# Performance work log

Hardware: AMD Instinct MI355X
Metric: run time of the kernel (lower is better)

The kernel has to match this reference:

```python
import jax, jax.numpy as jnp
from jax import lax
import numpy as np

N = 1024           # num_nodes
E = 32768          # edges per hop adjacency (avg degree 32)
EMB, HID, REP = 128, 64, 32
PATH_LENGTHS = (2, 3)


def _conv2d(x, w, b, pad):
    y = lax.conv_general_dilated(x, w, (1, 1), [(pad, pad), (pad, pad)],
                                 dimension_numbers=('NCHW', 'OIHW', 'NCHW'))
    return y + b[None, :, None, None]


def _tconv2d(x, w, b):
    # ConvTranspose2d(kernel=2, stride=2, pad=0) == conv with lhs_dilation=2, pad=1 (out = 2*in)
    y = lax.conv_general_dilated(x, w, (1, 1), [(1, 1), (1, 1)],
                                 lhs_dilation=(2, 2),
                                 dimension_numbers=('NCHW', 'OIHW', 'NCHW'))
    return y + b[None, :, None, None]


def _maxpool2(x):
    return lax.reduce_window(x, -jnp.inf, lax.max, (1, 1, 2, 2), (1, 1, 2, 2), 'VALID')


def _att_block(a, p):
    # ConvEncoder: conv->pool->conv->pool->tconv->tconv, relu/relu/relu/sigmoid
    h = jax.nn.relu(_conv2d(a, p[0], p[1], 1))
    h = _maxpool2(h)
    h = jax.nn.relu(_conv2d(h, p[2], p[3], 2))
    h = _maxpool2(h)
    h = jax.nn.relu(_tconv2d(h, p[4], p[5]))
    return jax.nn.sigmoid(_tconv2d(h, p[6], p[7]))


def _dense_gcn_norm(A):
    # add_remaining_self_loops(fill=1) + D^{-1/2} A D^{-1/2}; deg = row-sum (scatter_add over row)
    A = A + jnp.diag(jnp.where(jnp.diagonal(A) == 0, 1.0, 0.0).astype(A.dtype))
    deg = A.sum(axis=1)
    safe = jnp.where(deg > 0, deg, 1.0)
    dinv = jnp.where(deg > 0, lax.rsqrt(safe), 0.0)
    return dinv[:, None] * A * dinv[None, :]


def _edges_to_dense(e):
    # torch.sparse.FloatTensor(idx, ones).to_dense() sums duplicate edges
    return jnp.zeros((N, N), jnp.float32).at[e[0], e[1]].add(1.0)


def _path_transform(adjs, p):
    # adjs: [L, N, N] dense per-hop adjacencies of one meta-path
    att = _att_block(adjs[None], p)[0][:, :N, :N]
    attended = adjs * att
    M = jnp.eye(N, dtype=adjs.dtype)
    for i in range(adjs.shape[0]):  # fixed small loop over hops
        M = _dense_gcn_norm(M @ attended[i])
    return M


def _forward(x, p0, p1, w1, bias1, w2, bias2, e00, e01, e10, e11, e12):
    A0 = jnp.stack([_edges_to_dense(e00), _edges_to_dense(e01)])
    A1 = jnp.stack([_edges_to_dense(e10), _edges_to_dense(e11), _edges_to_dense(e12)])
    M0 = _path_transform(A0, p0)
    M1 = _path_transform(A1, p1)
    A = jnp.maximum(M0, M1)  # coalesce(op='max') over union; values are >= 0
    An = _dense_gcn_norm(A)  # GCNConv internal normalization (same for both layers)
    h = jax.nn.relu(An @ (x @ w1) + bias1)
    # dropout inactive (eval mode)
    return An @ (h @ w2) + bias2


def setup_inputs():
    key = jax.random.key(0)
    ks = iter(jax.random.split(key, 40))
    d = {}
    d['x'] = jax.random.normal(next(ks), (N, EMB), jnp.float32)
    d['mp0_e0'] = jax.random.randint(next(ks), (2, E), 0, N)
    d['mp0_e1'] = jax.random.randint(next(ks), (2, E), 0, N)
    d['mp1_e0'] = jax.random.randint(next(ks), (2, E), 0, N)
    d['mp1_e1'] = jax.random.randint(next(ks), (2, E), 0, N)
    d['mp1_e2'] = jax.random.randint(next(ks), (2, E), 0, N)
    for bi, L in enumerate(PATH_LENGTHS):
        pre = 'b%d_' % bi
        d[pre + 'c1w'] = jax.random.normal(next(ks), (16, L, 3, 3), jnp.float32) * 0.1
        d[pre + 'c1b'] = jnp.zeros((16,), jnp.float32)
        d[pre + 'c2w'] = jax.random.normal(next(ks), (4, 16, 3, 3), jnp.float32) * 0.1
        d[pre + 'c2b'] = jnp.zeros((4,), jnp.float32)
        d[pre + 't1w'] = jax.random.normal(next(ks), (16, 4, 2, 2), jnp.float32) * 0.1
        d[pre + 't1b'] = jnp.zeros((16,), jnp.float32)
        d[pre + 't2w'] = jax.random.normal(next(ks), (L, 16, 2, 2), jnp.float32) * 0.1
        d[pre + 't2b'] = jnp.zeros((L,), jnp.float32)
    d['w1'] = jax.random.normal(next(ks), (EMB, HID), jnp.float32) * (1.0 / np.sqrt(EMB)).astype(np.float32)
    d['bias1'] = jnp.zeros((HID,), jnp.float32)
    d['w2'] = jax.random.normal(next(ks), (HID, REP), jnp.float32) * (1.0 / np.sqrt(HID)).astype(np.float32)
    d['bias2'] = jnp.zeros((REP,), jnp.float32)
    return d


def reference(x, mp0_e0, mp0_e1, mp1_e0, mp1_e1, mp1_e2,
              b0_c1w, b0_c1b, b0_c2w, b0_c2b, b0_t1w, b0_t1b, b0_t2w, b0_t2b,
              b1_c1w, b1_c1b, b1_c2w, b1_c2b, b1_t1w, b1_t1b, b1_t2w, b1_t2b,
              w1, bias1, w2, bias2):
    p0 = (b0_c1w, b0_c1b, b0_c2w, b0_c2b, b0_t1w, b0_t1b, b0_t2w, b0_t2b)
    p1 = (b1_c1w, b1_c1b, b1_c2w, b1_c2b, b1_t1w, b1_t1b, b1_t2w, b1_t2b)
    return _forward(x, p0, p1, w1, bias1, w2, bias2,
                    mp0_e0, mp0_e1, mp1_e0, mp1_e1, mp1_e2)
```

## Files before the change

### kernel.cpp

```cpp
#include <hip/hip_runtime.h>
#include <math.h>

#define N 1024
#define NN (N*N)
#define NE 32768

#define OFF_A    ((size_t)0)
#define OFF_H10  ((size_t)(5*NN))
#define OFF_M0   ((size_t)(5*NN))
#define OFF_CSR  ((size_t)(7*NN))
#define OFF_BT   ((size_t)(9*NN))
#define OFF_M1   ((size_t)(10*NN))
#define OFF_AN   ((size_t)(11*NN))
#define OFF_H20  ((size_t)(13*NN))
#define OFF_H21  (OFF_H20 + 264196)
#define OFF_SC   (OFF_H21 + 264196)
#define SC_D0a 0
#define SC_F0a 1024
#define SC_D1a 2048
#define SC_F1a 3072
#define SC_D0b 4096
#define SC_F0b 5120
#define SC_D1b 6144
#define SC_F1b 7168
#define SC_D1c 8192
#define SC_F1c 9216
#define SC_D2  10240
#define SC_F2  11264
#define SC_DEG 12288
#define SC_DGV 13312
#define OFF_XW1  (OFF_SC + 14336)
#define OFF_HB   (OFF_XW1 + 65536)
#define OFF_HW2  (OFF_HB + 65536)

#define CSR_STRIDE 96
#define CSRF (1024 * CSR_STRIDE)
#define CSC_MAXT 80

__global__ void k_scatter5(const int* __restrict__ e0, const int* __restrict__ e1,
                           const int* __restrict__ e2, const int* __restrict__ e3,
                           const int* __restrict__ e4, float* __restrict__ A) {
  int g = blockIdx.x * 256 + threadIdx.x;
  int seg = g >> 15;
  int k = g & 32767;
  const int* e = (seg == 0) ? e0 : (seg == 1) ? e1 : (seg == 2) ? e2 : (seg == 3) ? e3 : e4;
  atomicAdd(&A[(size_t)seg * NN + (size_t)e[k] * N + e[NE + k]], 1.0f);
}

template<int L>
__device__ __forceinline__ void conv1_body(const float* __restrict__ A,
    const float* __restrict__ W, const float* __restrict__ Bn, float* __restrict__ out) {
  __shared__ float sIn[L][34][35];
  __shared__ float sW[16 * L * 9];
  __shared__ float sB[16];
  int tid = threadIdx.y * 16 + threadIdx.x;
  for (int i = tid; i < 16 * L * 9; i += 256) sW[i] = W[i];
  if (tid < 16) sB[tid] = Bn[tid];
  const int x0 = blockIdx.x * 32 - 1;
  const int y0 = blockIdx.y * 32 - 1;
  for (int idx = tid; idx < L * 34 * 34; idx += 256) {
    int l = idx / (34 * 34);
    int rem = idx - l * 34 * 34;
    int r = rem / 34, c = rem - r * 34;
    int iy = y0 + r, ix = x0 + c;
    sIn[l][r][c] = (iy >= 0 && iy < N && ix >= 0 && ix < N) ? A[(size_t)l * NN + (size_t)iy * N + ix] : 0.f;
  }
  __syncthreads();
  const int tx = threadIdx.x, ty = threadIdx.y;
  float p[L][4][4];
  #pragma unroll
  for (int l = 0; l < L; ++l)
    #pragma unroll
    for (int r = 0; r < 4; ++r)
      #pragma unroll
      for (int c = 0; c < 4; ++c)
        p[l][r][c] = sIn[l][2 * ty + r][2 * tx + c];
  const int ox = blockIdx.x * 16 + tx;
  const int oy = blockIdx.y * 16 + ty;
  for (int oc = 0; oc < 16; ++oc) {
    float wr[L * 9];
    #pragma unroll
    for (int t = 0; t < L * 9; ++t) wr[t] = sW[oc * L * 9 + t];
    float m = -1e30f;
    #pragma unroll
    for (int dy = 0; dy < 2; ++dy)
      #pragma unroll
      for (int dx = 0; dx < 2; ++dx) {
        float s = 0.f;
        #pragma unroll
        for (int l = 0; l < L; ++l)
          #pragma unroll
          for (int ky = 0; ky < 3; ++ky)
            #pragma unroll
            for (int kx = 0; kx < 3; ++kx)
              s = fmaf(p[l][dy + ky][dx + kx], wr[l * 9 + ky * 3 + kx], s);
        m = fmaxf(m, s);
      }
    out[(size_t)oc * 262144 + (size_t)oy * 512 + ox] = fmaxf(m + sB[oc], 0.f);
  }
}

__global__ __launch_bounds__(256) void k_conv1_both(const float* __restrict__ Ab,
    const float* __restrict__ W0, const float* __restrict__ b0,
    const float* __restrict__ W1, const float* __restrict__ b1, float* __restrict__ H1b) {
  if (blockIdx.z == 0) conv1_body<2>(Ab, W0, b0, H1b);
  else                 conv1_body<3>(Ab + 2 * NN, W1, b1, H1b + 4 * NN);
}

__global__ __launch_bounds__(256) void k_conv2_both(const float* __restrict__ H1b,
    const float* __restrict__ W0, const float* __restrict__ b0,
    const float* __restrict__ W1, const float* __restrict__ b1,
    float* __restrict__ H2_0, float* __restrict__ H2_1) {
  const int z = blockIdx.z;
  const float* in = H1b + (size_t)z * 4 * NN;
  const float* W  = z ? W1 : W0;
  const float* Bn = z ? b1 : b0;
  float* out = z ? H2_1 : H2_0;
  __shared__ float sW[4 * 16 * 9];
  __shared__ float sB[4];
  const int tid = threadIdx.x;
  for (int i = tid; i < 576; i += 256) sW[i] = W[i];
  if (tid < 4) sB[tid] = Bn[tid];
  __syncthreads();
  const int tx = tid & 15, ty = tid >> 4;
  const int ox = blockIdx.x * 16 + tx;
  const int oy = blockIdx.y * 16 + ty;
  if (ox >= 257 || oy >= 257) return;
  const int x0 = 2 * ox - 2;
  const int y0 = 2 * oy - 2;
  const bool c0ok = (x0 >= 0);
  const bool c1ok = (x0 + 2 < 512);
  float acc[4][2][2];
  #pragma unroll
  for (int oc = 0; oc < 4; ++oc)
    #pragma unroll
    for (int dy = 0; dy < 2; ++dy)
      #pragma unroll
      for (int dx = 0; dx < 2; ++dx) acc[oc][dy][dx] = 0.f;
  for (int ic = 0; ic < 16; ++ic) {
    const float* base = in + (size_t)ic * 262144;
    float p[4][4];
    #pragma unroll
    for (int r = 0; r < 4; ++r) {
      const int iy = y0 + r;
      const bool rowok = (iy >= 0 && iy < 512);
      float2 a = make_float2(0.f, 0.f), b = make_float2(0.f, 0.f);
      if (rowok) {
        const float* rp = base + (size_t)iy * 512;
        if (c0ok) a = *(const float2*)(rp + x0);
        if (c1ok) b = *(const float2*)(rp + x0 + 2);
      }
      p[r][0] = a.x; p[r][1] = a.y; p[r][2] = b.x; p[r][3] = b.y;
    }
    #pragma unroll
    for (int oc = 0; oc < 4; ++oc) {
      float wr[9];
      #pragma unroll
      for (int t = 0; t < 9; ++t) wr[t] = sW[oc * 144 + ic * 9 + t];
      #pragma unroll
      for (int ky = 0; ky < 3; ++ky)
        #pragma unroll
        for (int kx = 0; kx < 3; ++kx) {
          const float w = wr[ky * 3 + kx];
          #pragma unroll
          for (int dy = 0; dy < 2; ++dy)
            #pragma unroll
            for (int dx = 0; dx < 2; ++dx)
              acc[oc][dy][dx] = fmaf(p[dy + ky][dx + kx], w, acc[oc][dy][dx]);
        }
    }
  }
  #pragma unroll
  for (int oc = 0; oc < 4; ++oc) {
    float m = fmaxf(fmaxf(acc[oc][0][0], acc[oc][0][1]), fmaxf(acc[oc][1][0], acc[oc][1][1]));
    out[(size_t)oc * 66049 + (size_t)oy * 257 + ox] = fmaxf(m + sB[oc], 0.f);
  }
}

__global__ __launch_bounds__(256) void k_tc_both(
    const float* __restrict__ H2_0, const float* __restrict__ H2_1,
    const float* __restrict__ t1w0, const float* __restrict__ t1b0,
    const float* __restrict__ t2w0, const float* __restrict__ t2b0,
    const float* __restrict__ t1w1, const float* __restrict__ t1b1,
    const float* __restrict__ t2w1, const float* __restrict__ t2b1,
    float* __restrict__ Ab) {
  const int z = blockIdx.z;
  const int L = 2 + z;
  const float* in  = z ? H2_1 : H2_0;
  const float* W1p = z ? t1w1 : t1w0;
  const float* B1p = z ? t1b1 : t1b0;
  const float* W2p = z ? t2w1 : t2w0;
  const float* B2p = z ? t2b1 : t2b0;
  float* A = Ab + (size_t)z * 2 * NN;
  __shared__ float sW1[256], sB1[16], sW2[192], sB2[3];
  int tid = threadIdx.y * 16 + threadIdx.x;
  sW1[tid] = W1p[tid];
  if (tid < 16) sB1[tid] = B1p[tid];
  for (int i = tid; i < L * 64; i += 256) sW2[i] = W2p[i];
  if (tid < L) sB2[tid] = B2p[tid];
  __syncthreads();
  const int n = blockIdx.x * 16 + threadIdx.x;
  const int m = blockIdx.y * 16 + threadIdx.y;
  const int p = m >> 1, q = n >> 1;
  const int f1y = 1 - (m & 1), f1x = 1 - (n & 1);
  float vin[4];
  #pragma unroll
  for (int ci = 0; ci < 4; ++ci) vin[ci] = in[(size_t)ci * 66049 + (size_t)p * 257 + q];
  float v[16];
  #pragma unroll
  for (int c = 0; c < 16; ++c) {
    float s = sB1[c];
    #pragma unroll
    for (int ci = 0; ci < 4; ++ci)
      s = fmaf(vin[ci], sW1[c * 16 + ci * 4 + f1y * 2 + f1x], s);
    v[c] = fmaxf(s, 0.f);
  }
  for (int l = 0; l < L; ++l) {
    #pragma unroll
    for (int dy = 0; dy < 2; ++dy)
      #pragma unroll
      for (int dx = 0; dx < 2; ++dx) {
        float s = sB2[l];
        #pragma unroll
        for (int c = 0; c < 16; ++c)
          s = fmaf(v[c], sW2[l * 64 + c * 4 + (1 - dy) * 2 + (1 - dx)], s);
        float sg = 1.f / (1.f + expf(-s));
        size_t idx = (size_t)l * NN + (size_t)(2 * m + dy) * N + (2 * n + dx);
        A[idx] *= sg;
      }
  }
}

__global__ __launch_bounds__(256) void k_extract(const float* __restrict__ Ab,
    int* __restrict__ gcol, float* __restrict__ gval, int* __restrict__ gcnt,
    int* __restrict__ crowT, float* __restrict__ cvalT, int* __restrict__ ccnt,
    float* __restrict__ DEGACC,
    float* __restrict__ D0a, float* __restrict__ F0a,
    float* __restrict__ D1a, float* __restrict__ F1a) {
  const int row = blockIdx.x;
  const int y = blockIdx.y;
  const float* base = Ab + (size_t)y * NN + (size_t)row * N;
  __shared__ int cnt;
  __shared__ float sdiag;
  __shared__ float red[4];
  if (threadIdx.x == 0) cnt = 0;
  __syncthreads();
  const int j4 = threadIdx.x;
  float4 v = ((const float4*)base)[j4];
  if (j4 == (row >> 2)) sdiag = ((const float*)&v)[row & 3];
  if (y == 4) {
    if (threadIdx.x == 0) DEGACC[row] = 0.f;
    #pragma unroll
    for (int t = 0; t < 4; ++t) {
      float x = ((const float*)&v)[t];
      if (x != 0.f) {
        int j = 4 * j4 + t;
        int p = atomicAdd(&ccnt[j], 1);
        if (p < CSC_MAXT) { crowT[p * 1024 + j] = row; cvalT[p * 1024 + j] = x; }
      }
    }
    return;
  }
  const size_t rb = ((size_t)y * 1024 + row) * CSR_STRIDE;
  #pragma unroll
  for (int t = 0; t < 4; ++t) {
    float x = ((const float*)&v)[t];
    if (x != 0.f) {
      int p = atomicAdd(&cnt, 1);
      if (p < CSR_STRIDE) { gcol[rb + p] = 4 * j4 + t; gval[rb + p] = x; }
    }
  }
  float s = v.x + v.y + v.z + v.w;
  #pragma unroll
  for (int o = 32; o > 0; o >>= 1) s += __shfl_down(s, o, 64);
  if ((threadIdx.x & 63) == 0) red[threadIdx.x >> 6] = s;
  __syncthreads();
  if (threadIdx.x == 0) {
    gcnt[(size_t)y * 1024 + row] = (cnt < CSR_STRIDE) ? cnt : CSR_STRIDE;
    if (y == 0 || y == 2) {
      float tot = red[0] + red[1] + red[2] + red[3];
      float fl = (sdiag == 0.f) ? 1.f : 0.f;
      float deg = tot + fl;
      float* D = (y == 0) ? D0a : D1a;
      float* F = (y == 0) ? F0a : F1a;
      D[row] = (deg > 0.f) ? (1.f / sqrtf(deg)) : 0.f;
      F[row] = fl;
    }
  }
}

__global__ __launch_bounds__(256) void k_spmm(
    const int* __restrict__ gcol, const float* __restrict__ gval, const int* __restrict__ gcnt,
    const float* __restrict__ D0a, const float* __restrict__ F0a,
    const float* __restrict__ D1a, const float* __restrict__ F1a,
    float* __restrict__ M0, float* __restrict__ BT,
    float* __restrict__ D0b, float* __restrict__ F0b,
    float* __restrict__ D1b, float* __restrict__ F1b) {
  const int row = blockIdx.x;
  const int y = blockIdx.y;
  const int lm = y * 2, rm = y * 2 + 1;
  const float* Da = y ? D1a : D0a;
  const float* Fa = y ? F1a : F0a;
  __shared__ __align__(16) float acc[1024];
  __shared__ int lcol[112];
  __shared__ float lw[112];
  __shared__ int lrc[112];
  __shared__ int cl;
  __shared__ float red[4];
  __shared__ float sdiag;
  ((float4*)acc)[threadIdx.x] = make_float4(0.f, 0.f, 0.f, 0.f);
  const float di = Da[row];
  const int cnt_l = gcnt[(size_t)lm * 1024 + row];
  const size_t lb = ((size_t)lm * 1024 + row) * CSR_STRIDE;
  if (threadIdx.x < cnt_l) {
    int k = gcol[lb + threadIdx.x];
    lcol[threadIdx.x] = k;
    lw[threadIdx.x] = di * gval[lb + threadIdx.x] * Da[k];
    lrc[threadIdx.x] = gcnt[(size_t)rm * 1024 + k];
  }
  if (threadIdx.x == 0) {
    int c = cnt_l;
    if (Fa[row] != 0.f) {
      lcol[c] = row; lw[c] = di * di; lrc[c] = gcnt[(size_t)rm * 1024 + row]; ++c;
    }
    cl = c;
  }
  __syncthreads();
  const int sub = threadIdx.x >> 5, lane = threadIdx.x & 31;
  const int cle = cl;
  for (int e = sub; e < cle; e += 8) {
    const int k = lcol[e];
    const float w = lw[e];
    const int rc = lrc[e];
    const size_t rbv = ((size_t)rm * 1024 + k) * CSR_STRIDE;
    for (int t = lane; t < rc; t += 32)
      atomicAdd(&acc[gcol[rbv + t]], w * gval[rbv + t]);
  }
  __syncthreads();
  float4 o = ((const float4*)acc)[threadIdx.x];
  float* C = y ? BT : M0;
  ((float4*)(C + (size_t)row * N))[threadIdx.x] = o;
  if (threadIdx.x == (row >> 2)) sdiag = ((const float*)&o)[row & 3];
  float s = o.x + o.y + o.z + o.w;
  #pragma unroll
  for (int off = 32; off > 0; off >>= 1) s += __shfl_down(s, off, 64);
  if ((threadIdx.x & 63) == 0) red[threadIdx.x >> 6] = s;
  __syncthreads();
  if (threadIdx.x == 0) {
    float tot = red[0] + red[1] + red[2] + red[3];
    float fl = (sdiag == 0.f) ? 1.f : 0.f;
    float deg = tot + fl;
    float* D = y ? D1b : D0b;
    float* F = y ? F1b : F0b;
    D[row] = (deg > 0.f) ? (1.f / sqrtf(deg)) : 0.f;
    F[row] = fl;
  }
}

__global__ __launch_bounds__(256) void k_spmm2(const float* __restrict__ BT,
    const float* __restrict__ D1b, const float* __restrict__ F1b,
    const int* __restrict__ crowT, const float* __restrict__ cvalT, const int* __restrict__ ccnt,
    float* __restrict__ M1, float* __restrict__ DEGACC, float* __restrict__ DIAGV) {
  const int g0 = blockIdx.x << 3;
  const int j  = (blockIdx.y << 8) + threadIdx.x;
  __shared__ float bt[1024 * 9];
  __shared__ float wsum[4][8];
  const int tid = threadIdx.x;
  for (int kq = 0; kq < 4; ++kq) {
    const int k = (kq << 8) + tid;
    const float dv = D1b[k];
    #pragma unroll
    for (int row = 0; row < 8; ++row)
      bt[k * 9 + row] = BT[(size_t)(g0 + row) * N + k] * dv;
  }
  __syncthreads();
  if (tid < 8) {
    const int gr = g0 + tid;
    bt[gr * 9 + tid] += F1b[gr] * D1b[gr];
  }
  __syncthreads();
  int cn = ccnt[j];
  cn = min(cn, CSC_MAXT);
  float o[8];
  #pragma unroll
  for (int row = 0; row < 8; ++row) o[row] = 0.f;
  for (int t = 0; t < cn; ++t) {
    const int   r = crowT[t * 1024 + j];
    const float v = cvalT[t * 1024 + j];
    const int rb = r * 9;
    #pragma unroll
    for (int row = 0; row < 8; ++row)
      o[row] = fmaf(bt[rb + row], v, o[row]);
  }
  #pragma unroll
  for (int row = 0; row < 8; ++row) o[row] *= D1b[g0 + row];
  #pragma unroll
  for (int row = 0; row < 8; ++row)
    M1[(size_t)(g0 + row) * N + j] = o[row];
  if ((unsigned)(j - g0) < 8u) DIAGV[j] = o[j - g0];
  #pragma unroll
  for (int row = 0; row < 8; ++row) {
    float s = o[row];
    #pragma unroll
    for (int off = 32; off > 0; off >>= 1) s += __shfl_down(s, off, 64);
    if ((tid & 63) == 0) wsum[tid >> 6][row] = s;
  }
  __syncthreads();
  if (tid < 8) {
    float p = wsum[0][tid] + wsum[1][tid] + wsum[2][tid] + wsum[3][tid];
    atomicAdd(&DEGACC[g0 + tid], p);
  }
}

__global__ void k_fin(const float* __restrict__ DEGACC, const float* __restrict__ DIAGV,
                      float* __restrict__ D1c, float* __restrict__ F1c) {
  const int row = blockIdx.x * 256 + threadIdx.x;
  const float fl = (DIAGV[row] == 0.f) ? 1.f : 0.f;
  const float deg = DEGACC[row] + fl;
  D1c[row] = (deg > 0.f) ? (1.f / sqrtf(deg)) : 0.f;
  F1c[row] = fl;
}

__global__ __launch_bounds__(256) void k_maxdeg(const float* __restrict__ M0,
    const float* __restrict__ d0, const float* __restrict__ f0,
    const float* __restrict__ M1, const float* __restrict__ d1, const float* __restrict__ f1,
    float* __restrict__ Aout, float* __restrict__ dinv2, float* __restrict__ dflg2) {
  const int row = blockIdx.x;
  const int j4 = threadIdx.x;
  const float r0 = d0[row], r1 = d1[row];
  const float fl0 = f0[row], fl1 = f1[row];
  float4 a = ((const float4*)(M0 + (size_t)row * N))[j4];
  float4 b = ((const float4*)(M1 + (size_t)row * N))[j4];
  const float4 c0 = ((const float4*)d0)[j4];
  const float4 c1 = ((const float4*)d1)[j4];
  int d = row - 4 * j4;
  if ((unsigned)d < 4u) { ((float*)&a)[d] += fl0; ((float*)&b)[d] += fl1; }
  float4 o;
  o.x = fmaxf(a.x * r0 * c0.x, b.x * r1 * c1.x);
  o.y = fmaxf(a.y * r0 * c0.y, b.y * r1 * c1.y);
  o.z = fmaxf(a.z * r0 * c0.z, b.z * r1 * c1.z);
  o.w = fmaxf(a.w * r0 * c0.w, b.w * r1 * c1.w);
  ((float4*)(Aout + (size_t)row * N))[j4] = o;
  __shared__ float sdiag;
  if ((unsigned)d < 4u) sdiag = ((float*)&o)[d];
  float s = o.x + o.y + o.z + o.w;
  #pragma unroll
  for (int off = 32; off > 0; off >>= 1) s += __shfl_down(s, off, 64);
  __shared__ float red[4];
  if ((threadIdx.x & 63) == 0) red[threadIdx.x >> 6] = s;
  __syncthreads();
  if (threadIdx.x == 0) {
    float tot = red[0] + red[1] + red[2] + red[3];
    float fl = (sdiag == 0.0f) ? 1.0f : 0.0f;
    float deg = tot + fl;
    dinv2[row] = (deg > 0.0f) ? (1.0f / sqrtf(deg)) : 0.0f;
    dflg2[row] = fl;
  }
}

template<int K, int NCOL, bool BIAS, bool RELU>
__global__ void k_mm_small(const float* __restrict__ A, const float* __restrict__ B,
                           const float* __restrict__ bias, float* __restrict__ out) {
  const int j = threadIdx.x;
  const int i = blockIdx.x * blockDim.y + threadIdx.y;
  const float* ar = A + (size_t)i * K;
  float acc = 0.f;
  #pragma unroll 8
  for (int k = 0; k < K; ++k) acc = fmaf(ar[k], B[(size_t)k * NCOL + j], acc);
  if (BIAS) acc += bias[j];
  if (RELU) acc = fmaxf(acc, 0.f);
  out[(size_t)i * NCOL + j] = acc;
}

template<int NCOL, bool RELU>
__global__ void k_an_mm(const float* __restrict__ BT, const float* __restrict__ dinv,
                        const float* __restrict__ dflg, const float* __restrict__ Bm,
                        const float* __restrict__ bias, float* __restrict__ out) {
  const int j = threadIdx.x;
  const int i = blockIdx.x * blockDim.y + threadIdx.y;
  const float di = dinv[i];
  const float* ar = BT + (size_t)i * N;
  float acc = 0.f;
  for (int k = 0; k < N; k += 4) {
    float4 a4 = *(const float4*)&ar[k];
    float4 d4 = *(const float4*)&dinv[k];
    acc = fmaf(a4.x * d4.x, Bm[(size_t)(k + 0) * NCOL + j], acc);
    acc = fmaf(a4.y * d4.y, Bm[(size_t)(k + 1) * NCOL + j], acc);
    acc = fmaf(a4.z * d4.z, Bm[(size_t)(k + 2) * NCOL + j], acc);
    acc = fmaf(a4.w * d4.w, Bm[(size_t)(k + 3) * NCOL + j], acc);
  }
  acc = fmaf(dflg[i] * dinv[i], Bm[(size_t)i * NCOL + j], acc);
  acc = fmaf(di, acc, bias[j]);
  if (RELU) acc = fmaxf(acc, 0.f);
  out[(size_t)i * NCOL + j] = acc;
}

extern "C" void kernel_launch(void* const* d_in, const int* in_sizes, int n_in,
                              void* d_out, int out_size, void* d_ws, size_t ws_size,
                              hipStream_t stream) {
  const float* x     = (const float*)d_in[0];
  const float* w1    = (const float*)d_in[22];
  const float* bias1 = (const float*)d_in[23];
  const float* w2    = (const float*)d_in[24];
  const float* bias2 = (const float*)d_in[25];
  float* out = (float*)d_out;
  float* ws  = (float*)d_ws;

  float* A    = ws + OFF_A;
  float* H1   = ws + OFF_H10;
  float* M0   = ws + OFF_M0;
  float* BT   = ws + OFF_BT;
  float* M1   = ws + OFF_M1;
  float* AN   = ws + OFF_AN;
  float* H2_0 = ws + OFF_H20;
  float* H2_1 = ws + OFF_H21;
  int*   gcol  = (int*)(ws + OFF_CSR);
  float* gval  = ws + OFF_CSR + (size_t)4 * CSRF;
  int*   gcnt  = (int*)(ws + OFF_CSR + (size_t)8 * CSRF);
  int*   crowT = (int*)(ws + OFF_CSR + (size_t)8 * CSRF + 4096);
  float* cvalT = ws + OFF_CSR + (size_t)8 * CSRF + 4096 + CSC_MAXT * 1024;
  int*   ccnt  = (int*)(ws + OFF_CSR + (size_t)8 * CSRF + 4096 + (size_t)2 * CSC_MAXT * 1024);
  float* SC   = ws + OFF_SC;
  float *D0a = SC + SC_D0a, *F0a = SC + SC_F0a, *D1a = SC + SC_D1a, *F1a = SC + SC_F1a;
  float *D0b = SC + SC_D0b, *F0b = SC + SC_F0b, *D1b = SC + SC_D1b, *F1b = SC + SC_F1b;
  float *D1c = SC + SC_D1c, *F1c = SC + SC_F1c, *D2 = SC + SC_D2, *F2 = SC + SC_F2;
  float *DEGACC = SC + SC_DEG, *DIAGV = SC + SC_DGV;
  float* XW1 = ws + OFF_XW1;
  float* HB  = ws + OFF_HB;
  float* HW2 = ws + OFF_HW2;

  hipMemsetAsync(A, 0, (size_t)5 * NN * sizeof(float), stream);

  dim3 b256(256), b16(16, 16);
  k_mm_small<128, 64, false, false><<<256, dim3(64, 4), 0, stream>>>(x, w1, nullptr, XW1);

  k_scatter5<<<640, b256, 0, stream>>>((const int*)d_in[1], (const int*)d_in[2],
                                       (const int*)d_in[3], (const int*)d_in[4],
                                       (const int*)d_in[5], A);

  k_conv1_both<<<dim3(32, 32, 2), b16, 0, stream>>>(A,
      (const float*)d_in[6], (const float*)d_in[7],
      (const float*)d_in[14], (const float*)d_in[15], H1);
  k_conv2_both<<<dim3(17, 17, 2), b256, 0, stream>>>(H1,
      (const float*)d_in[8], (const float*)d_in[9],
      (const float*)d_in[16], (const float*)d_in[17], H2_0, H2_1);
  k_tc_both<<<dim3(32, 32, 2), b16, 0, stream>>>(H2_0, H2_1,
      (const float*)d_in[10], (const float*)d_in[11],
      (const float*)d_in[12], (const float*)d_in[13],
      (const float*)d_in[18], (const float*)d_in[19],
      (const float*)d_in[20], (const float*)d_in[21], A);

  hipMemsetAsync(ccnt, 0, 1024 * sizeof(int), stream);

  k_extract<<<dim3(1024, 5), b256, 0, stream>>>(A, gcol, gval, gcnt,
      crowT, cvalT, ccnt, DEGACC, D0a, F0a, D1a, F1a);

  k_spmm<<<dim3(1024, 2), b256, 0, stream>>>(gcol, gval, gcnt,
      D0a, F0a, D1a, F1a, M0, BT, D0b, F0b, D1b, F1b);

  k_spmm2<<<dim3(128, 4), b256, 0, stream>>>(BT, D1b, F1b, crowT, cvalT, ccnt,
                                             M1, DEGACC, DIAGV);
  k_fin<<<4, b256, 0, stream>>>(DEGACC, DIAGV, D1c, F1c);

  k_maxdeg<<<1024, b256, 0, stream>>>(M0, D0b, F0b, M1, D1c, F1c, AN, D2, F2);

  k_an_mm<64, true><<<256, dim3(64, 4), 0, stream>>>(AN, D2, F2, XW1, bias1, HB);
  k_mm_small<64, 32, false, false><<<128, dim3(32, 8), 0, stream>>>(HB, w2, nullptr, HW2);
  k_an_mm<32, false><<<128, dim3(32, 8), 0, stream>>>(AN, D2, F2, HW2, bias2, out);
}
```

Baseline: 369.1 us.

## Fuse sparse extraction into transposed-conv epilogue and merge small GEMM stages

The attention-apply kernel now emits CSR/CSC entries, degree sums and diagonals directly while multiplying the adjacency by the sigmoid attention. This removes the separate pass that re-read the five dense 1024x1024 matrices. Zeroing of the counters moves into the first conv block, which drops a memset. The final-norm kernel is folded into k_maxdeg, and the second hidden GEMM is fused with the layer-1 aggregation. The cost is global atomics per nonzero on the row counters and degree sums, and nondeterministic ordering inside each CSR row.

```diff
diff --git a/kernel.cpp b/kernel.cpp
--- a/kernel.cpp
+++ b/kernel.cpp
@@ -15,23 +15,26 @@
 #define OFF_H20  ((size_t)(13*NN))
 #define OFF_H21  (OFF_H20 + 264196)
 #define OFF_SC   (OFF_H21 + 264196)
-#define SC_D0a 0
-#define SC_F0a 1024
-#define SC_D1a 2048
-#define SC_F1a 3072
-#define SC_D0b 4096
-#define SC_F0b 5120
-#define SC_D1b 6144
-#define SC_F1b 7168
-#define SC_D1c 8192
-#define SC_F1c 9216
-#define SC_D2  10240
-#define SC_F2  11264
-#define SC_DEG 12288
-#define SC_DGV 13312
-#define OFF_XW1  (OFF_SC + 14336)
-#define OFF_HB   (OFF_XW1 + 65536)
-#define OFF_HW2  (OFF_HB + 65536)
+#define SC_D0a   0
+#define SC_F0a   1024
+#define SC_D1a   2048
+#define SC_F1a   3072
+#define SC_D0b   4096
+#define SC_F0b   5120
+#define SC_D1b   6144
+#define SC_F1b   7168
+#define SC_D2    8192
+#define SC_F2    9216
+#define SC_ZERO  10240
+#define SC_DEG   10240
+#define SC_GCNT  11264
+#define SC_CCNT  15360
+#define SC_DEGA  16384
+#define SC_DIAGA 18432
+#define SC_DGV   20480
+#define SC_END   21504
+#define OFF_XW1  (OFF_SC + SC_END)
+#define OFF_HW2  (OFF_XW1 + 65536)
 
 #define CSR_STRIDE 96
 #define CSRF (1024 * CSR_STRIDE)
@@ -102,7 +105,12 @@
 
 __global__ __launch_bounds__(256) void k_conv1_both(const float* __restrict__ Ab,
     const float* __restrict__ W0, const float* __restrict__ b0,
-    const float* __restrict__ W1, const float* __restrict__ b1, float* __restrict__ H1b) {
+    const float* __restrict__ W1, const float* __restrict__ b1,
+    float* __restrict__ H1b, float* __restrict__ ZC) {
+  if (blockIdx.x == 0 && blockIdx.y == 0 && blockIdx.z == 0) {
+    int tid = threadIdx.y * 16 + threadIdx.x;
+    for (int i = tid; i < 10240; i += 256) ZC[i] = 0.f;
+  }
   if (blockIdx.z == 0) conv1_body<2>(Ab, W0, b0, H1b);
   else                 conv1_body<3>(Ab + 2 * NN, W1, b1, H1b + 4 * NN);
 }
@@ -177,13 +185,16 @@
   }
 }
 
-__global__ __launch_bounds__(256) void k_tc_both(
+__global__ __launch_bounds__(256) void k_tc_emit(
     const float* __restrict__ H2_0, const float* __restrict__ H2_1,
     const float* __restrict__ t1w0, const float* __restrict__ t1b0,
     const float* __restrict__ t2w0, const float* __restrict__ t2b0,
     const float* __restrict__ t1w1, const float* __restrict__ t1b1,
     const float* __restrict__ t2w1, const float* __restrict__ t2b1,
-    float* __restrict__ Ab) {
+    const float* __restrict__ Ab,
+    int* __restrict__ gcolA, float* __restrict__ gvalA, int* __restrict__ gcntA,
+    int* __restrict__ crowT, float* __restrict__ cvalT, int* __restrict__ ccnt,
+    float* __restrict__ DEGA, float* __restrict__ DIAGA) {
   const int z = blockIdx.z;
   const int L = 2 + z;
   const float* in  = z ? H2_1 : H2_0;
@@ -191,7 +202,6 @@
   const float* B1p = z ? t1b1 : t1b0;
   const float* W2p = z ? t2w1 : t2w0;
   const float* B2p = z ? t2b1 : t2b0;
-  float* A = Ab + (size_t)z * 2 * NN;
   __shared__ float sW1[256], sB1[16], sW2[192], sB2[3];
   int tid = threadIdx.y * 16 + threadIdx.x;
   sW1[tid] = W1p[tid];
@@ -206,16 +216,17 @@
   float vin[4];
   #pragma unroll
   for (int ci = 0; ci < 4; ++ci) vin[ci] = in[(size_t)ci * 66049 + (size_t)p * 257 + q];
-  float v[16];
+  float v16[16];
   #pragma unroll
   for (int c = 0; c < 16; ++c) {
     float s = sB1[c];
     #pragma unroll
     for (int ci = 0; ci < 4; ++ci)
       s = fmaf(vin[ci], sW1[c * 16 + ci * 4 + f1y * 2 + f1x], s);
-    v[c] = fmaxf(s, 0.f);
+    v16[c] = fmaxf(s, 0.f);
   }
   for (int l = 0; l < L; ++l) {
+    const int mat = z * 2 + l;
     #pragma unroll
     for (int dy = 0; dy < 2; ++dy)
       #pragma unroll
@@ -223,70 +234,41 @@
         float s = sB2[l];
         #pragma unroll
         for (int c = 0; c < 16; ++c)
-          s = fmaf(v[c], sW2[l * 64 + c * 4 + (1 - dy) * 2 + (1 - dx)], s);
-        float sg = 1.f / (1.f + expf(-s));
-        size_t idx = (size_t)l * NN + (size_t)(2 * m + dy) * N + (2 * n + dx);
-        A[idx] *= sg;
+          s = fmaf(v16[c], sW2[l * 64 + c * 4 + (1 - dy) * 2 + (1 - dx)], s);
+        const float sg = 1.f / (1.f + expf(-s));
+        const int grow = 2 * m + dy, gc = 2 * n + dx;
+        const float av = Ab[(size_t)mat * NN + (size_t)grow * N + gc];
+        const float v = av * sg;
+        if (v != 0.f) {
+          if (mat == 4) {
+            int pp = atomicAdd(&ccnt[gc], 1);
+            if (pp < CSC_MAXT) { crowT[pp * 1024 + gc] = grow; cvalT[pp * 1024 + gc] = v; }
+          } else {
+            int pp = atomicAdd(&gcntA[mat * 1024 + grow], 1);
+            if (pp < CSR_STRIDE) {
+              size_t rb = ((size_t)mat * 1024 + grow) * CSR_STRIDE;
+              gcolA[rb + pp] = gc; gvalA[rb + pp] = v;
+            }
+          }
+          if (mat == 0 || mat == 2) {
+            atomicAdd(&DEGA[(mat >> 1) * 1024 + grow], v);
+            if (grow == gc) DIAGA[(mat >> 1) * 1024 + grow] = v;
+          }
+        }
       }
   }
 }
 
-__global__ __launch_bounds__(256) void k_extract(const float* __restrict__ Ab,
-    int* __restrict__ gcol, float* __restrict__ gval, int* __restrict__ gcnt,
-    int* __restrict__ crowT, float* __restrict__ cvalT, int* __restrict__ ccnt,
-    float* __restrict__ DEGACC,
+__global__ void k_finA(const float* __restrict__ DEGA, const float* __restrict__ DIAGA,
     float* __restrict__ D0a, float* __restrict__ F0a,
     float* __restrict__ D1a, float* __restrict__ F1a) {
-  const int row = blockIdx.x;
-  const int y = blockIdx.y;
-  const float* base = Ab + (size_t)y * NN + (size_t)row * N;
-  __shared__ int cnt;
-  __shared__ float sdiag;
-  __shared__ float red[4];
-  if (threadIdx.x == 0) cnt = 0;
-  __syncthreads();
-  const int j4 = threadIdx.x;
-  float4 v = ((const float4*)base)[j4];
-  if (j4 == (row >> 2)) sdiag = ((const float*)&v)[row & 3];
-  if (y == 4) {
-    if (threadIdx.x == 0) DEGACC[row] = 0.f;
-    #pragma unroll
-    for (int t = 0; t < 4; ++t) {
-      float x = ((const float*)&v)[t];
-      if (x != 0.f) {
-        int j = 4 * j4 + t;
-        int p = atomicAdd(&ccnt[j], 1);
-        if (p < CSC_MAXT) { crowT[p * 1024 + j] = row; cvalT[p * 1024 + j] = x; }
-      }
-    }
-    return;
-  }
-  const size_t rb = ((size_t)y * 1024 + row) * CSR_STRIDE;
-  #pragma unroll
-  for (int t = 0; t < 4; ++t) {
-    float x = ((const float*)&v)[t];
-    if (x != 0.f) {
-      int p = atomicAdd(&cnt, 1);
-      if (p < CSR_STRIDE) { gcol[rb + p] = 4 * j4 + t; gval[rb + p] = x; }
-    }
-  }
-  float s = v.x + v.y + v.z + v.w;
-  #pragma unroll
-  for (int o = 32; o > 0; o >>= 1) s += __shfl_down(s, o, 64);
-  if ((threadIdx.x & 63) == 0) red[threadIdx.x >> 6] = s;
-  __syncthreads();
-  if (threadIdx.x == 0) {
-    gcnt[(size_t)y * 1024 + row] = (cnt < CSR_STRIDE) ? cnt : CSR_STRIDE;
-    if (y == 0 || y == 2) {
-      float tot = red[0] + red[1] + red[2] + red[3];
-      float fl = (sdiag == 0.f) ? 1.f : 0.f;
-      float deg = tot + fl;
-      float* D = (y == 0) ? D0a : D1a;
-      float* F = (y == 0) ? F0a : F1a;
-      D[row] = (deg > 0.f) ? (1.f / sqrtf(deg)) : 0.f;
-      F[row] = fl;
-    }
-  }
+  const int i = blockIdx.x * 256 + threadIdx.x;
+  const int which = i >> 10, row = i & 1023;
+  const float fl = (DIAGA[i] == 0.f) ? 1.f : 0.f;
+  const float deg = DEGA[i] + fl;
+  const float d = (deg > 0.f) ? (1.f / sqrtf(deg)) : 0.f;
+  if (which == 0) { D0a[row] = d; F0a[row] = fl; }
+  else            { D1a[row] = d; F1a[row] = fl; }
 }
 
 __global__ __launch_bounds__(256) void k_spmm(
@@ -310,18 +292,19 @@
   __shared__ float sdiag;
   ((float4*)acc)[threadIdx.x] = make_float4(0.f, 0.f, 0.f, 0.f);
   const float di = Da[row];
-  const int cnt_l = gcnt[(size_t)lm * 1024 + row];
+  const int cnt_l = min(gcnt[(size_t)lm * 1024 + row], CSR_STRIDE);
   const size_t lb = ((size_t)lm * 1024 + row) * CSR_STRIDE;
   if (threadIdx.x < cnt_l) {
     int k = gcol[lb + threadIdx.x];
     lcol[threadIdx.x] = k;
     lw[threadIdx.x] = di * gval[lb + threadIdx.x] * Da[k];
-    lrc[threadIdx.x] = gcnt[(size_t)rm * 1024 + k];
+    lrc[threadIdx.x] = min(gcnt[(size_t)rm * 1024 + k], CSR_STRIDE);
   }
   if (threadIdx.x == 0) {
     int c = cnt_l;
     if (Fa[row] != 0.f) {
-      lcol[c] = row; lw[c] = di * di; lrc[c] = gcnt[(size_t)rm * 1024 + row]; ++c;
+      lcol[c] = row; lw[c] = di * di;
+      lrc[c] = min(gcnt[(size_t)rm * 1024 + row], CSR_STRIDE); ++c;
     }
     cl = c;
   }
@@ -412,27 +395,34 @@
   }
 }
 
-__global__ void k_fin(const float* __restrict__ DEGACC, const float* __restrict__ DIAGV,
-                      float* __restrict__ D1c, float* __restrict__ F1c) {
-  const int row = blockIdx.x * 256 + threadIdx.x;
-  const float fl = (DIAGV[row] == 0.f) ? 1.f : 0.f;
-  const float deg = DEGACC[row] + fl;
-  D1c[row] = (deg > 0.f) ? (1.f / sqrtf(deg)) : 0.f;
-  F1c[row] = fl;
-}
-
 __global__ __launch_bounds__(256) void k_maxdeg(const float* __restrict__ M0,
     const float* __restrict__ d0, const float* __restrict__ f0,
-    const float* __restrict__ M1, const float* __restrict__ d1, const float* __restrict__ f1,
+    const float* __restrict__ M1,
+    const float* __restrict__ DEGACC, const float* __restrict__ DIAGV,
     float* __restrict__ Aout, float* __restrict__ dinv2, float* __restrict__ dflg2) {
   const int row = blockIdx.x;
   const int j4 = threadIdx.x;
-  const float r0 = d0[row], r1 = d1[row];
-  const float fl0 = f0[row], fl1 = f1[row];
+  const float r0 = d0[row], fl0 = f0[row];
+  const float flr = (DIAGV[row] == 0.f) ? 1.f : 0.f;
+  const float degr = DEGACC[row] + flr;
+  const float r1 = (degr > 0.f) ? (1.f / sqrtf(degr)) : 0.f;
+  const float fl1 = flr;
   float4 a = ((const float4*)(M0 + (size_t)row * N))[j4];
   float4 b = ((const float4*)(M1 + (size_t)row * N))[j4];
   const float4 c0 = ((const float4*)d0)[j4];
-  const float4 c1 = ((const float4*)d1)[j4];
+  const float4 da = ((const float4*)DEGACC)[j4];
+  const float4 gv = ((const float4*)DIAGV)[j4];
+  float4 c1;
+  {
+    float fx = (gv.x == 0.f) ? 1.f : 0.f, dx_ = da.x + fx;
+    float fy = (gv.y == 0.f) ? 1.f : 0.f, dy_ = da.y + fy;
+    float fz = (gv.z == 0.f) ? 1.f : 0.f, dz_ = da.z + fz;
+    float fw = (gv.w == 0.f) ? 1.f : 0.f, dw_ = da.w + fw;
+    c1.x = (dx_ > 0.f) ? (1.f / sqrtf(dx_)) : 0.f;
+    c1.y = (dy_ > 0.f) ? (1.f / sqrtf(dy_)) : 0.f;
+    c1.z = (dz_ > 0.f) ? (1.f / sqrtf(dz_)) : 0.f;
+    c1.w = (dw_ > 0.f) ? (1.f / sqrtf(dw_)) : 0.f;
+  }
   int d = row - 4 * j4;
   if ((unsigned)d < 4u) { ((float*)&a)[d] += fl0; ((float*)&b)[d] += fl1; }
   float4 o;
@@ -470,6 +460,38 @@
   if (BIAS) acc += bias[j];
   if (RELU) acc = fmaxf(acc, 0.f);
   out[(size_t)i * NCOL + j] = acc;
+}
+
+__global__ void k_an_mm1(const float* __restrict__ AN, const float* __restrict__ dinv,
+                         const float* __restrict__ dflg, const float* __restrict__ XW1,
+                         const float* __restrict__ bias1, const float* __restrict__ w2,
+                         float* __restrict__ HW2) {
+  __shared__ float hsh[4][64];
+  const int j = threadIdx.x;
+  const int ty = threadIdx.y;
+  const int i = blockIdx.x * 4 + ty;
+  const float di = dinv[i];
+  const float* ar = AN + (size_t)i * N;
+  float acc = 0.f;
+  for (int k = 0; k < N; k += 4) {
+    float4 a4 = *(const float4*)&ar[k];
+    float4 d4 = *(const float4*)&dinv[k];
+    acc = fmaf(a4.x * d4.x, XW1[(size_t)(k + 0) * 64 + j], acc);
+    acc = fmaf(a4.y * d4.y, XW1[(size_t)(k + 1) * 64 + j], acc);
+    acc = fmaf(a4.z * d4.z, XW1[(size_t)(k + 2) * 64 + j], acc);
+    acc = fmaf(a4.w * d4.w, XW1[(size_t)(k + 3) * 64 + j], acc);
+  }
+  acc = fmaf(dflg[i] * dinv[i], XW1[(size_t)i * 64 + j], acc);
+  acc = fmaf(di, acc, bias1[j]);
+  acc = fmaxf(acc, 0.f);
+  hsh[ty][j] = acc;
+  __syncthreads();
+  if (j < 32) {
+    float s = 0.f;
+    #pragma unroll 8
+    for (int k2 = 0; k2 < 64; ++k2) s = fmaf(hsh[ty][k2], w2[k2 * 32 + j], s);
+    HW2[(size_t)i * 32 + j] = s;
+  }
 }
 
 template<int NCOL, bool RELU>
@@ -516,17 +538,18 @@
   float* H2_1 = ws + OFF_H21;
   int*   gcol  = (int*)(ws + OFF_CSR);
   float* gval  = ws + OFF_CSR + (size_t)4 * CSRF;
-  int*   gcnt  = (int*)(ws + OFF_CSR + (size_t)8 * CSRF);
-  int*   crowT = (int*)(ws + OFF_CSR + (size_t)8 * CSRF + 4096);
-  float* cvalT = ws + OFF_CSR + (size_t)8 * CSRF + 4096 + CSC_MAXT * 1024;
-  int*   ccnt  = (int*)(ws + OFF_CSR + (size_t)8 * CSRF + 4096 + (size_t)2 * CSC_MAXT * 1024);
+  int*   crowT = (int*)(ws + OFF_CSR + (size_t)8 * CSRF);
+  float* cvalT = ws + OFF_CSR + (size_t)8 * CSRF + CSC_MAXT * 1024;
   float* SC   = ws + OFF_SC;
   float *D0a = SC + SC_D0a, *F0a = SC + SC_F0a, *D1a = SC + SC_D1a, *F1a = SC + SC_F1a;
   float *D0b = SC + SC_D0b, *F0b = SC + SC_F0b, *D1b = SC + SC_D1b, *F1b = SC + SC_F1b;
-  float *D1c = SC + SC_D1c, *F1c = SC + SC_F1c, *D2 = SC + SC_D2, *F2 = SC + SC_F2;
+  float *D2 = SC + SC_D2, *F2 = SC + SC_F2;
   float *DEGACC = SC + SC_DEG, *DIAGV = SC + SC_DGV;
+  int*   gcnt = (int*)(SC + SC_GCNT);
+  int*   ccnt = (int*)(SC + SC_CCNT);
+  float *DEGA = SC + SC_DEGA, *DIAGA = SC + SC_DIAGA;
+  float* ZC   = SC + SC_ZERO;
   float* XW1 = ws + OFF_XW1;
-  float* HB  = ws + OFF_HB;
   float* HW2 = ws + OFF_HW2;
 
   hipMemsetAsync(A, 0, (size_t)5 * NN * sizeof(float), stream);
@@ -540,31 +563,27 @@
 
   k_conv1_both<<<dim3(32, 32, 2), b16, 0, stream>>>(A,
       (const float*)d_in[6], (const float*)d_in[7],
-      (const float*)d_in[14], (const float*)d_in[15], H1);
+      (const float*)d_in[14], (const float*)d_in[15], H1, ZC);
   k_conv2_both<<<dim3(17, 17, 2), b256, 0, stream>>>(H1,
       (const float*)d_in[8], (const float*)d_in[9],
       (const float*)d_in[16], (const float*)d_in[17], H2_0, H2_1);
-  k_tc_both<<<dim3(32, 32, 2), b16, 0, stream>>>(H2_0, H2_1,
+
+  k_tc_emit<<<dim3(32, 32, 2), b16, 0, stream>>>(H2_0, H2_1,
       (const float*)d_in[10], (const float*)d_in[11],
       (const float*)d_in[12], (const float*)d_in[13],
       (const float*)d_in[18], (const float*)d_in[19],
-      (const float*)d_in[20], (const float*)d_in[21], A);
-
-  hipMemsetAsync(ccnt, 0, 1024 * sizeof(int), stream);
-
-  k_extract<<<dim3(1024, 5), b256, 0, stream>>>(A, gcol, gval, gcnt,
-      crowT, cvalT, ccnt, DEGACC, D0a, F0a, D1a, F1a);
+      (const float*)d_in[20], (const float*)d_in[21],
+      A, gcol, gval, gcnt, crowT, cvalT, ccnt, DEGA, DIAGA);
+  k_finA<<<8, b256, 0, stream>>>(DEGA, DIAGA, D0a, F0a, D1a, F1a);
 
   k_spmm<<<dim3(1024, 2), b256, 0, stream>>>(gcol, gval, gcnt,
       D0a, F0a, D1a, F1a, M0, BT, D0b, F0b, D1b, F1b);
 
   k_spmm2<<<dim3(128, 4), b256, 0, stream>>>(BT, D1b, F1b, crowT, cvalT, ccnt,
                                              M1, DEGACC, DIAGV);
-  k_fin<<<4, b256, 0, stream>>>(DEGACC, DIAGV, D1c, F1c);
-
-  k_maxdeg<<<1024, b256, 0, stream>>>(M0, D0b, F0b, M1, D1c, F1c, AN, D2, F2);
-
-  k_an_mm<64, true><<<256, dim3(64, 4), 0, stream>>>(AN, D2, F2, XW1, bias1, HB);
-  k_mm_small<64, 32, false, false><<<128, dim3(32, 8), 0, stream>>>(HB, w2, nullptr, HW2);
+
+  k_maxdeg<<<1024, b256, 0, stream>>>(M0, D0b, F0b, M1, DEGACC, DIAGV, AN, D2, F2);
+
+  k_an_mm1<<<256, dim3(64, 4), 0, stream>>>(AN, D2, F2, XW1, bias1, w2, HW2);
   k_an_mm<32, false><<<128, dim3(32, 8), 0, stream>>>(AN, D2, F2, HW2, bias2, out);
 }
```

Result: faster. 343.0 us (-7.1%).
